# Kernel tuning notes

Hardware: AMD Instinct MI355X
Metric: run time of the kernel (lower is better)

## Reference

```python
import jax, jax.numpy as jnp
import numpy as np

MAX_LEN = 366

def _pe_table(d_model, max_len=MAX_LEN):
    # standard sinusoidal positional encoding table [max_len, d_model]
    pos = jnp.arange(max_len, dtype=jnp.float32)[:, None]
    div = jnp.exp(jnp.arange(0, d_model, 2, dtype=jnp.float32) * (-jnp.log(10000.0) / d_model))
    ang = pos * div  # [max_len, d_model/2]
    pe = jnp.zeros((max_len, d_model), dtype=jnp.float32)
    pe = pe.at[:, 0::2].set(jnp.sin(ang))
    pe = pe.at[:, 1::2].set(jnp.cos(ang))
    return pe

def setup_inputs() -> dict:
    key = jax.random.key(0)
    k1, k2, k3, k4 = jax.random.split(key, 4)
    B, S, F, D = 1024, 128, 10, 256
    input_sequence = jax.random.normal(k1, (B, S, F), dtype=jnp.float32)
    doy_sequence = jnp.sort(jax.random.randint(k2, (B, S), 0, MAX_LEN), axis=-1)
    W = jax.random.normal(k3, (D, F), dtype=jnp.float32) * (1.0 / np.sqrt(F))
    b = jax.random.normal(k4, (D,), dtype=jnp.float32) * 0.01
    return {"input_sequence": input_sequence, "doy_sequence": doy_sequence, "W": W, "b": b}

def reference(input_sequence, doy_sequence, W, b):
    # obs_embed: linear projection of per-observation features  [B,S,D]
    obs_embed = jnp.einsum('bsf,df->bsd', input_sequence, W) + b
    D = W.shape[0]
    pe = _pe_table(D)[doy_sequence]  # vectorized gather over the whole batch [B,S,D]
    # original: x = obs_embed.repeat(1,1,2) then overwrite second half with PE
    out = jnp.concatenate([obs_embed, pe], axis=-1)  # [B,S,2D]
    # dropout is identity in eval mode
    return out
```

## Files before the change

### kernel.cpp

```cpp
#include <hip/hip_runtime.h>


#define CHUNK  32
#define BLKPOS 128

__global__ __launch_bounds__(256) void bert_embed_kernel(
    const float* __restrict__ x,
    const int*   __restrict__ doy,
    const float* __restrict__ W,
    const float* __restrict__ bvec,
    float*       __restrict__ out,
    int BS)
{
    __shared__ float lx[BLKPOS * 10];
    __shared__ float ldoyf[BLKPOS];

    const int tid  = threadIdx.x;
    const int lane = tid & 63;
    const int wave = tid >> 6;
    const int blk_base = blockIdx.x * BLKPOS;
    if (blk_base >= BS) return;

    const int valid = min(BLKPOS, BS - blk_base);

    if (valid == BLKPOS) {
        const float4* xb  = (const float4*)(x + (size_t)blk_base * 10);
        float4*       lx4 = (float4*)lx;
        int idx = tid;
        lx4[idx] = xb[idx];
        idx += 256;
        if (idx < 320) lx4[idx] = xb[idx];
    } else {
        for (int i = tid; i < valid * 10; i += 256)
            lx[i] = x[(size_t)blk_base * 10 + i];
    }
    if (tid < valid) ldoyf[tid] = (float)doy[blk_base + tid];

    const int d0 = lane * 4;
    float wf[40];
    {
        const float4* wp = (const float4*)(W + (size_t)d0 * 10);
        #pragma unroll
        for (int c = 0; c < 10; ++c) {
            float4 v = wp[c];
            wf[4 * c + 0] = v.x; wf[4 * c + 1] = v.y;
            wf[4 * c + 2] = v.z; wf[4 * c + 3] = v.w;
        }
    }
    const float4 bv = *(const float4*)(bvec + d0);

    const float e0 = __builtin_amdgcn_exp2f(
        fmaf((float)(2 * lane + 0), -0.10381025296522976f, -2.651496129472319f));
    const float e1 = __builtin_amdgcn_exp2f(
        fmaf((float)(2 * lane + 1), -0.10381025296522976f, -2.651496129472319f));

    __syncthreads();

    const int wbase = wave * CHUNK;
    const int n = min(CHUNK, valid - wbase);
    float* o = out + ((size_t)blk_base + wbase) * 512 + d0;

    #pragma unroll 2
    for (int it = 0; it < n; ++it) {
        const float* xr = lx + (wbase + it) * 10;
        float xf[10];
        #pragma unroll
        for (int c = 0; c < 5; ++c) {
            float2 v = *(const float2*)(xr + 2 * c);
            xf[2 * c]     = v.x;
            xf[2 * c + 1] = v.y;
        }
        const float pos = ldoyf[wbase + it];

        float acc0 = bv.x, acc1 = bv.y, acc2 = bv.z, acc3 = bv.w;
        #pragma unroll
        for (int f = 0; f < 10; ++f) {
            acc0 = fmaf(xf[f], wf[ 0 + f], acc0);
            acc1 = fmaf(xf[f], wf[10 + f], acc1);
            acc2 = fmaf(xf[f], wf[20 + f], acc2);
            acc3 = fmaf(xf[f], wf[30 + f], acc3);
        }

        float r0 = pos * e0;
        float r1 = pos * e1;
        r0 -= floorf(r0);
        r1 -= floorf(r1);
        float4 s1 = { __builtin_amdgcn_sinf(r0), __builtin_amdgcn_cosf(r0),
                      __builtin_amdgcn_sinf(r1), __builtin_amdgcn_cosf(r1) };
        float4 s0 = { acc0, acc1, acc2, acc3 };

        *(float4*)(o)       = s0;
        *(float4*)(o + 256) = s1;
        o += 512;
    }
}

extern "C" void kernel_launch(void* const* d_in, const int* in_sizes, int n_in,
                              void* d_out, int out_size, void* d_ws, size_t ws_size,
                              hipStream_t stream) {
    const float* x    = (const float*)d_in[0];
    const int*   doy  = (const int*)d_in[1];
    const float* W    = (const float*)d_in[2];
    const float* bvec = (const float*)d_in[3];
    float*       out  = (float*)d_out;

    const int BS = in_sizes[1];
    const int blocks = (BS + BLKPOS - 1) / BLKPOS;
    bert_embed_kernel<<<blocks, 256, 0, stream>>>(x, doy, W, bvec, out, BS);
}
```

Before: 266.5 us.

## Halve block size, stage W transposed in LDS, prefetch rows, use nontemporal stores

Halves positions per block (BLKPOS 64, CHUNK 16), which doubles the number of blocks. W is now loaded coalesced into a transposed LDS tile, replacing strided per-lane global loads, and each wave software-prefetches the next row's features and day-of-year from LDS. Output writes become nontemporal stores to avoid polluting the cache with the large streaming output. The trade-off is that every block reloads the full 10KB W into LDS, which adds per-block overhead, and LDS use grows.

Measured after the change: 269.3 us. No clear change (+1.0%).

```diff
diff --git a/kernel.cpp b/kernel.cpp
--- a/kernel.cpp
+++ b/kernel.cpp
@@ -1,8 +1,10 @@
 #include <hip/hip_runtime.h>
 
 
-#define CHUNK  32
-#define BLKPOS 128
+#define CHUNK  16
+#define BLKPOS 64
+
+typedef float f32x4 __attribute__((ext_vector_type(4)));
 
 __global__ __launch_bounds__(256) void bert_embed_kernel(
     const float* __restrict__ x,
@@ -12,6 +14,7 @@
     float*       __restrict__ out,
     int BS)
 {
+    __shared__ float lwt[10 * 256];
     __shared__ float lx[BLKPOS * 10];
     __shared__ float ldoyf[BLKPOS];
 
@@ -20,16 +23,16 @@
     const int wave = tid >> 6;
     const int blk_base = blockIdx.x * BLKPOS;
     if (blk_base >= BS) return;
-
     const int valid = min(BLKPOS, BS - blk_base);
 
+    {
+        const float* wr = W + (size_t)tid * 10;
+        #pragma unroll
+        for (int f = 0; f < 10; ++f) lwt[f * 256 + tid] = wr[f];
+    }
     if (valid == BLKPOS) {
-        const float4* xb  = (const float4*)(x + (size_t)blk_base * 10);
-        float4*       lx4 = (float4*)lx;
-        int idx = tid;
-        lx4[idx] = xb[idx];
-        idx += 256;
-        if (idx < 320) lx4[idx] = xb[idx];
+        const f32x4* xb = (const f32x4*)(x + (size_t)blk_base * 10);
+        if (tid < 160) ((f32x4*)lx)[tid] = xb[tid];
     } else {
         for (int i = tid; i < valid * 10; i += 256)
             lx[i] = x[(size_t)blk_base * 10 + i];
@@ -37,17 +40,7 @@
     if (tid < valid) ldoyf[tid] = (float)doy[blk_base + tid];
 
     const int d0 = lane * 4;
-    float wf[40];
-    {
-        const float4* wp = (const float4*)(W + (size_t)d0 * 10);
-        #pragma unroll
-        for (int c = 0; c < 10; ++c) {
-            float4 v = wp[c];
-            wf[4 * c + 0] = v.x; wf[4 * c + 1] = v.y;
-            wf[4 * c + 2] = v.z; wf[4 * c + 3] = v.w;
-        }
-    }
-    const float4 bv = *(const float4*)(bvec + d0);
+    const f32x4 bv = *(const f32x4*)(bvec + d0);
 
     const float e0 = __builtin_amdgcn_exp2f(
         fmaf((float)(2 * lane + 0), -0.10381025296522976f, -2.651496129472319f));
@@ -56,21 +49,43 @@
 
     __syncthreads();
 
+    float wf[40];
+    #pragma unroll
+    for (int f = 0; f < 10; ++f) {
+        f32x4 v = *(const f32x4*)(lwt + f * 256 + d0);
+        wf[ 0 + f] = v.x;
+        wf[10 + f] = v.y;
+        wf[20 + f] = v.z;
+        wf[30 + f] = v.w;
+    }
+
     const int wbase = wave * CHUNK;
     const int n = min(CHUNK, valid - wbase);
+    if (n <= 0) return;
     float* o = out + ((size_t)blk_base + wbase) * 512 + d0;
 
-    #pragma unroll 2
-    for (int it = 0; it < n; ++it) {
-        const float* xr = lx + (wbase + it) * 10;
-        float xf[10];
+    float xf[10]; float posv;
+    {
+        const float* xr = lx + wbase * 10;
         #pragma unroll
         for (int c = 0; c < 5; ++c) {
             float2 v = *(const float2*)(xr + 2 * c);
-            xf[2 * c]     = v.x;
-            xf[2 * c + 1] = v.y;
+            xf[2 * c] = v.x; xf[2 * c + 1] = v.y;
         }
-        const float pos = ldoyf[wbase + it];
+        posv = ldoyf[wbase];
+    }
+
+    for (int it = 0; it < n; ++it) {
+        float xn[10]; float posn = 0.0f;
+        if (it + 1 < n) {
+            const float* xr = lx + (wbase + it + 1) * 10;
+            #pragma unroll
+            for (int c = 0; c < 5; ++c) {
+                float2 v = *(const float2*)(xr + 2 * c);
+                xn[2 * c] = v.x; xn[2 * c + 1] = v.y;
+            }
+            posn = ldoyf[wbase + it + 1];
+        }
 
         float acc0 = bv.x, acc1 = bv.y, acc2 = bv.z, acc3 = bv.w;
         #pragma unroll
@@ -81,17 +96,23 @@
             acc3 = fmaf(xf[f], wf[30 + f], acc3);
         }
 
-        float r0 = pos * e0;
-        float r1 = pos * e1;
+        float r0 = posv * e0;
+        float r1 = posv * e1;
         r0 -= floorf(r0);
         r1 -= floorf(r1);
-        float4 s1 = { __builtin_amdgcn_sinf(r0), __builtin_amdgcn_cosf(r0),
-                      __builtin_amdgcn_sinf(r1), __builtin_amdgcn_cosf(r1) };
-        float4 s0 = { acc0, acc1, acc2, acc3 };
+        f32x4 s1 = { __builtin_amdgcn_sinf(r0), __builtin_amdgcn_cosf(r0),
+                     __builtin_amdgcn_sinf(r1), __builtin_amdgcn_cosf(r1) };
+        f32x4 s0 = { acc0, acc1, acc2, acc3 };
 
-        *(float4*)(o)       = s0;
-        *(float4*)(o + 256) = s1;
+        __builtin_nontemporal_store(s0, (f32x4*)(o));
+        __builtin_nontemporal_store(s1, (f32x4*)(o + 256));
         o += 512;
+
+        if (it + 1 < n) {
+            #pragma unroll
+            for (int k = 0; k < 10; ++k) xf[k] = xn[k];
+            posv = posn;
+        }
     }
 }
 
```
